# Kernel optimization log

Measured on AMD Instinct MI355X. Metric: run time of the kernel, lower is better.

Reference implementation:

```python
import jax, jax.numpy as jnp
import numpy as np

N_NODES = 100000
N_EDGES = 3200000
D_IN = 256
D_OUT = 256


def setup_inputs() -> dict:
    key = jax.random.key(0)
    k1, k2, k3, k4, k5 = jax.random.split(key, 5)
    # kaiming-uniform-like init for weight
    bound = float(np.sqrt(6.0 / D_IN))
    weight = jax.random.uniform(k1, (D_IN, D_OUT), dtype=jnp.float32, minval=-bound, maxval=bound)
    bias = jnp.zeros((D_OUT,), dtype=jnp.float32)
    input_feature = jax.random.normal(k2, (N_NODES, D_IN), dtype=jnp.float32)
    # sparse_poly in COO form: (row, col, val), typical normalized graph polynomial values
    edge_row = jax.random.randint(k3, (N_EDGES,), 0, N_NODES, dtype=jnp.int32)
    edge_col = jax.random.randint(k4, (N_EDGES,), 0, N_NODES, dtype=jnp.int32)
    edge_val = jax.random.uniform(k5, (N_EDGES,), dtype=jnp.float32)
    return {
        "input_feature": input_feature,
        "weight": weight,
        "bias": bias,
        "edge_val": edge_val,
        "edge_row": edge_row,
        "edge_col": edge_col,
    }


def reference(input_feature, weight, bias, edge_val, edge_row, edge_col):
    # support = X @ W  -> [N, D_OUT]
    support = input_feature @ weight
    # output = sparse_poly @ support  (COO SpMM):
    # gather source rows, scale by edge values, scatter-add into destination rows
    messages = edge_val[:, None] * support[edge_col]  # [E, D_OUT]
    output = jax.ops.segment_sum(messages, edge_row, num_segments=N_NODES)
    return output + bias
```

## Files before the change

### kernel.cpp

```cpp
#include <hip/hip_runtime.h>

#define D 256
#define GBM 128
#define WT_PITCH 264
#define BSH 9
#define RPB 512
#define NBMAX 256
#define TILE 4096

using bf16x8 = __attribute__((ext_vector_type(8))) short;
using f32x4  = __attribute__((ext_vector_type(4))) float;

static __device__ __forceinline__ unsigned short f2bf(float f) {
    unsigned u = __builtin_bit_cast(unsigned, f);
    return (unsigned short)((u + 0x7fffu + ((u >> 16) & 1u)) >> 16);
}
static __device__ __forceinline__ float as_f(unsigned u) {
    return __builtin_bit_cast(float, u);
}

__global__ void wt_kernel(const float* __restrict__ W, unsigned short* __restrict__ Wt) {
    int idx = blockIdx.x * blockDim.x + threadIdx.x;
    int n = idx & 255, k = idx >> 8;
    Wt[n * 256 + k] = f2bf(W[k * 256 + n]);
}

__global__ __launch_bounds__(512) void gemm_mfma(const float* __restrict__ X,
                                                 const unsigned short* __restrict__ Wt,
                                                 unsigned short* __restrict__ S, int N) {
    __shared__ unsigned short wlds[256 * WT_PITCH];

    for (int c = threadIdx.x; c < 8192; c += 512) {
        int n = c >> 5, kc = c & 31;
        uint4 v = *reinterpret_cast<const uint4*>(Wt + n * 256 + kc * 8);
        *reinterpret_cast<uint4*>(&wlds[n * WT_PITCH + kc * 8]) = v;
    }
    __syncthreads();

    const int lane = threadIdx.x & 63;
    const int wave = threadIdx.x >> 6;
    const int row0 = blockIdx.x * GBM + wave * 16;
    const int l16  = lane & 15;
    const int kgrp = lane >> 4;
    const int arow = min(row0 + l16, N - 1);
    const float* xp = X + (size_t)arow * 256 + kgrp * 8;

    f32x4 acc[16];
#pragma unroll
    for (int i = 0; i < 16; i++) acc[i] = (f32x4)(0.0f);

#pragma unroll
    for (int ks = 0; ks < 8; ks++) {
        float4 a0 = *reinterpret_cast<const float4*>(xp + ks * 32);
        float4 a1 = *reinterpret_cast<const float4*>(xp + ks * 32 + 4);
        bf16x8 af;
        af[0] = (short)f2bf(a0.x); af[1] = (short)f2bf(a0.y);
        af[2] = (short)f2bf(a0.z); af[3] = (short)f2bf(a0.w);
        af[4] = (short)f2bf(a1.x); af[5] = (short)f2bf(a1.y);
        af[6] = (short)f2bf(a1.z); af[7] = (short)f2bf(a1.w);
#pragma unroll
        for (int nt = 0; nt < 16; nt++) {
            bf16x8 bf = *reinterpret_cast<const bf16x8*>(
                &wlds[(nt * 16 + l16) * WT_PITCH + ks * 32 + kgrp * 8]);
            acc[nt] = __builtin_amdgcn_mfma_f32_16x16x32_bf16(af, bf, acc[nt], 0, 0, 0);
        }
    }

#pragma unroll
    for (int nt = 0; nt < 16; nt++) {
#pragma unroll
        for (int j = 0; j < 4; j++) {
            int r = row0 + kgrp * 4 + j;
            if (r < N) S[(size_t)r * 256 + nt * 16 + l16] = f2bf(acc[nt][j]);
        }
    }
}

__global__ __launch_bounds__(256) void bucket_hist(const int* __restrict__ rows,
                                                   int* __restrict__ bcounts,
                                                   int E, int NB) {
    __shared__ int lh[NBMAX];
    for (int i = threadIdx.x; i < NB; i += 256) lh[i] = 0;
    __syncthreads();
    const int stride = gridDim.x * 256;
    for (int e = blockIdx.x * 256 + threadIdx.x; e < E; e += stride)
        atomicAdd(&lh[rows[e] >> BSH], 1);
    __syncthreads();
    for (int i = threadIdx.x; i < NB; i += 256) {
        int v = lh[i];
        if (v) atomicAdd(&bcounts[i], v);
    }
}

__global__ __launch_bounds__(1024) void bscan_kernel(const int* __restrict__ bcounts,
                                                     int* __restrict__ boffs,
                                                     int* __restrict__ bcursor, int NB) {
    __shared__ int wsum[16];
    const int t = threadIdx.x, lane = t & 63, w = t >> 6;
    int x = (t < NB) ? bcounts[t] : 0;
    int s = x;
#pragma unroll
    for (int d = 1; d < 64; d <<= 1) {
        int y = __shfl_up(s, d);
        if (lane >= d) s += y;
    }
    if (lane == 63) wsum[w] = s;
    __syncthreads();
    if (w == 0) {
        int ws = (lane < 16) ? wsum[lane] : 0;
#pragma unroll
        for (int d = 1; d < 16; d <<= 1) {
            int y = __shfl_up(ws, d);
            if (lane >= d) ws += y;
        }
        if (lane < 16) wsum[lane] = ws;
    }
    __syncthreads();
    int excl = (w ? wsum[w - 1] : 0) + s - x;
    if (t < NB) { boffs[t] = excl; bcursor[t] = excl; }
}

__global__ __launch_bounds__(256) void partition_kernel(const int* __restrict__ rows,
                                                        const int* __restrict__ cols,
                                                        const float* __restrict__ vals,
                                                        int* __restrict__ bcursor,
                                                        int2* __restrict__ packed,
                                                        int E, int NB) {
    __shared__ int lh[NBMAX];
    __shared__ int gbase[NBMAX];
    const int t = threadIdx.x;
    const int e0 = blockIdx.x * TILE;

    for (int i = t; i < NB; i += 256) lh[i] = 0;
    __syncthreads();

    int bk[16], rk[16], pc[16], pv[16];
#pragma unroll
    for (int j = 0; j < 16; j++) {
        int idx = e0 + j * 256 + t;
        if (idx < E) {
            int r = rows[idx];
            bk[j] = r >> BSH;
            rk[j] = atomicAdd(&lh[bk[j]], 1);
            pc[j] = ((r & (RPB - 1)) << 17) | cols[idx];
            pv[j] = __float_as_int(vals[idx]);
        } else {
            bk[j] = -1;
        }
    }
    __syncthreads();

    for (int i = t; i < NB; i += 256) {
        int c = lh[i];
        gbase[i] = c ? atomicAdd(&bcursor[i], c) : 0;
    }
    __syncthreads();

#pragma unroll
    for (int j = 0; j < 16; j++) {
        if (bk[j] >= 0) {
            int2 p; p.x = pc[j]; p.y = pv[j];
            packed[(size_t)gbase[bk[j]] + rk[j]] = p;
        }
    }
}

__global__ __launch_bounds__(256) void bucket_scatter(const int2* __restrict__ packed,
                                                      const int* __restrict__ boffs,
                                                      const int* __restrict__ bcounts,
                                                      int* __restrict__ offs,
                                                      int* __restrict__ counts,
                                                      int2* __restrict__ cv, int N) {
    __shared__ int cnt[RPB];
    __shared__ int lofs[RPB];
    __shared__ int wsum[4];
    const int b = blockIdx.x, t = threadIdx.x;
    const int base = boffs[b], nb = bcounts[b];

    for (int i = t; i < RPB; i += 256) cnt[i] = 0;
    __syncthreads();
    for (int i = t; i < nb; i += 256)
        atomicAdd(&cnt[((unsigned)packed[base + i].x) >> 17], 1);
    __syncthreads();

    const int lane = t & 63, w = t >> 6;
    int a0 = cnt[2 * t], a1 = cnt[2 * t + 1];
    int s = a0 + a1;
    int ss = s;
#pragma unroll
    for (int d = 1; d < 64; d <<= 1) {
        int y = __shfl_up(ss, d);
        if (lane >= d) ss += y;
    }
    if (lane == 63) wsum[w] = ss;
    __syncthreads();
    int wex = 0;
    if (w > 0) wex += wsum[0];
    if (w > 1) wex += wsum[1];
    if (w > 2) wex += wsum[2];
    int excl = wex + ss - s;

    const int r0 = b << BSH;
    int r = r0 + 2 * t;
    if (r < N)     { offs[r]     = base + excl;      counts[r]     = a0; }
    if (r + 1 < N) { offs[r + 1] = base + excl + a0; counts[r + 1] = a1; }
    lofs[2 * t]     = excl;
    lofs[2 * t + 1] = excl + a0;
    __syncthreads();

    for (int i = t; i < nb; i += 256) {
        int2 p = packed[base + i];
        int lr = ((unsigned)p.x) >> 17;
        int pos = base + atomicAdd(&lofs[lr], 1);
        int2 o;
        o.x = p.x & 0x1FFFF;
        o.y = p.y;
        cv[pos] = o;
    }
}

__global__ __launch_bounds__(256) void spmm_kernel(const unsigned short* __restrict__ S,
                                                   const int* __restrict__ offs,
                                                   const int* __restrict__ counts,
                                                   const int2* __restrict__ cv,
                                                   const float* __restrict__ bias,
                                                   float* __restrict__ out, int N) {
    const int lane = threadIdx.x & 63;
    const int r = blockIdx.x * 4 + (threadIdx.x >> 6);
    if (r >= N) return;
    const char* Sb = reinterpret_cast<const char*>(S);

    float4 acc = { 0.f, 0.f, 0.f, 0.f };
    int i = offs[r];
    const int end = i + counts[r];

#define GATHER(c, v)                                                              \
    {                                                                             \
        uint2 sv = *reinterpret_cast<const uint2*>(Sb + ((size_t)(c) << 9) + (lane << 3)); \
        acc.x += (v) * as_f(sv.x << 16);                                          \
        acc.y += (v) * as_f(sv.x & 0xffff0000u);                                  \
        acc.z += (v) * as_f(sv.y << 16);                                          \
        acc.w += (v) * as_f(sv.y & 0xffff0000u);                                  \
    }

    for (; i + 3 < end; i += 4) {
        int2 e0 = cv[i], e1 = cv[i + 1], e2 = cv[i + 2], e3 = cv[i + 3];
        GATHER(e0.x, as_f((unsigned)e0.y));
        GATHER(e1.x, as_f((unsigned)e1.y));
        GATHER(e2.x, as_f((unsigned)e2.y));
        GATHER(e3.x, as_f((unsigned)e3.y));
    }
    for (; i < end; i++) {
        int2 e0 = cv[i];
        GATHER(e0.x, as_f((unsigned)e0.y));
    }
#undef GATHER

    float4 b = reinterpret_cast<const float4*>(bias)[lane];
    float4 o = { acc.x + b.x, acc.y + b.y, acc.z + b.z, acc.w + b.w };
    reinterpret_cast<float4*>(out)[(size_t)r * 64 + lane] = o;
}

extern "C" void kernel_launch(void* const* d_in, const int* in_sizes, int n_in,
                              void* d_out, int out_size, void* d_ws, size_t ws_size,
                              hipStream_t stream) {
    const float* X     = (const float*)d_in[0];
    const float* W     = (const float*)d_in[1];
    const float* bias  = (const float*)d_in[2];
    const float* evals = (const float*)d_in[3];
    const int*   erow  = (const int*)d_in[4];
    const int*   ecol  = (const int*)d_in[5];
    float* out = (float*)d_out;

    const int N = in_sizes[0] / D;
    const int E = in_sizes[3];
    const int NB = (N + RPB - 1) >> BSH;

    char* ws = (char*)d_ws;
    size_t off = 0;
    auto alloc = [&](size_t bytes) {
        void* p = ws + off;
        off += (bytes + 255) & ~(size_t)255;
        return p;
    };
    unsigned short* S  = (unsigned short*)alloc((size_t)N * D * sizeof(unsigned short));
    unsigned short* Wt = (unsigned short*)alloc((size_t)D * D * sizeof(unsigned short));
    int* bcounts = (int*)alloc((size_t)NB * sizeof(int));
    int* boffs   = (int*)alloc((size_t)NB * sizeof(int));
    int* bcursor = (int*)alloc((size_t)NB * sizeof(int));
    int* offs    = (int*)alloc((size_t)N * sizeof(int));
    int* counts  = (int*)alloc((size_t)N * sizeof(int));
    int2* packed = (int2*)alloc((size_t)E * sizeof(int2));
    int2* cv     = (int2*)alloc((size_t)E * sizeof(int2));

    wt_kernel<<<(D * D) / 256, 256, 0, stream>>>(W, Wt);
    gemm_mfma<<<(N + GBM - 1) / GBM, 512, 0, stream>>>(X, Wt, S, N);
    hipMemsetAsync(bcounts, 0, (size_t)NB * sizeof(int), stream);
    bucket_hist<<<1024, 256, 0, stream>>>(erow, bcounts, E, NB);
    bscan_kernel<<<1, 1024, 0, stream>>>(bcounts, boffs, bcursor, NB);
    partition_kernel<<<(E + TILE - 1) / TILE, 256, 0, stream>>>(erow, ecol, evals, bcursor,
                                                                packed, E, NB);
    bucket_scatter<<<NB, 256, 0, stream>>>(packed, boffs, bcounts, offs, counts, cv, N);
    spmm_kernel<<<(N + 3) / 4, 256, 0, stream>>>(S, offs, counts, cv, bias, out, N);
}
```

Measured before the change: 413.2 us.

## Drop GEMM LDS staging, fold memset, widen bucket scatter and unroll SpMM

The GEMM no longer stages the bf16 weight into a 135KB shared-memory tile. Each wave now reads B fragments straight from global/L2, and blocks shrink to 256 threads covering 64 rows, which should let more blocks fit per CU. The bcounts memset is folded into wt_kernel, bucket_scatter runs 1024 threads with a two-level scan, and the SpMM gather loop is unrolled by 8 to put more loads in flight. The risk is heavier L2 traffic for the weight reads in the GEMM.

```diff
diff --git a/kernel.cpp b/kernel.cpp
--- a/kernel.cpp
+++ b/kernel.cpp
@@ -1,7 +1,6 @@
 #include <hip/hip_runtime.h>
 
 #define D 256
-#define GBM 128
 #define WT_PITCH 264
 #define BSH 9
 #define RPB 512
@@ -19,31 +18,25 @@
     return __builtin_bit_cast(float, u);
 }
 
-__global__ void wt_kernel(const float* __restrict__ W, unsigned short* __restrict__ Wt) {
+__global__ void wt_kernel(const float* __restrict__ W, unsigned short* __restrict__ Wt,
+                          int* __restrict__ bcounts, int NB) {
     int idx = blockIdx.x * blockDim.x + threadIdx.x;
     int n = idx & 255, k = idx >> 8;
     Wt[n * 256 + k] = f2bf(W[k * 256 + n]);
-}
-
-__global__ __launch_bounds__(512) void gemm_mfma(const float* __restrict__ X,
+    if (blockIdx.x == 0 && threadIdx.x < NB) bcounts[threadIdx.x] = 0;
+}
+
+__global__ __launch_bounds__(256) void gemm_mfma(const float* __restrict__ X,
                                                  const unsigned short* __restrict__ Wt,
                                                  unsigned short* __restrict__ S, int N) {
-    __shared__ unsigned short wlds[256 * WT_PITCH];
-
-    for (int c = threadIdx.x; c < 8192; c += 512) {
-        int n = c >> 5, kc = c & 31;
-        uint4 v = *reinterpret_cast<const uint4*>(Wt + n * 256 + kc * 8);
-        *reinterpret_cast<uint4*>(&wlds[n * WT_PITCH + kc * 8]) = v;
-    }
-    __syncthreads();
-
     const int lane = threadIdx.x & 63;
     const int wave = threadIdx.x >> 6;
-    const int row0 = blockIdx.x * GBM + wave * 16;
+    const int row0 = blockIdx.x * 64 + wave * 16;
     const int l16  = lane & 15;
     const int kgrp = lane >> 4;
     const int arow = min(row0 + l16, N - 1);
     const float* xp = X + (size_t)arow * 256 + kgrp * 8;
+    const unsigned short* wp = Wt + l16 * 256 + kgrp * 8;
 
     f32x4 acc[16];
 #pragma unroll
@@ -61,7 +54,7 @@
 #pragma unroll
         for (int nt = 0; nt < 16; nt++) {
             bf16x8 bf = *reinterpret_cast<const bf16x8*>(
-                &wlds[(nt * 16 + l16) * WT_PITCH + ks * 32 + kgrp * 8]);
+                wp + nt * 16 * 256 + ks * 32);
             acc[nt] = __builtin_amdgcn_mfma_f32_16x16x32_bf16(af, bf, acc[nt], 0, 0, 0);
         }
     }
@@ -165,50 +158,55 @@
     }
 }
 
-__global__ __launch_bounds__(256) void bucket_scatter(const int2* __restrict__ packed,
-                                                      const int* __restrict__ boffs,
-                                                      const int* __restrict__ bcounts,
-                                                      int* __restrict__ offs,
-                                                      int* __restrict__ counts,
-                                                      int2* __restrict__ cv, int N) {
+__global__ __launch_bounds__(1024) void bucket_scatter(const int2* __restrict__ packed,
+                                                       const int* __restrict__ boffs,
+                                                       const int* __restrict__ bcounts,
+                                                       int* __restrict__ offs,
+                                                       int* __restrict__ counts,
+                                                       int2* __restrict__ cv, int N) {
     __shared__ int cnt[RPB];
     __shared__ int lofs[RPB];
-    __shared__ int wsum[4];
+    __shared__ int wsum[16];
     const int b = blockIdx.x, t = threadIdx.x;
     const int base = boffs[b], nb = bcounts[b];
-
-    for (int i = t; i < RPB; i += 256) cnt[i] = 0;
-    __syncthreads();
-    for (int i = t; i < nb; i += 256)
+    const int lane = t & 63, w = t >> 6;
+
+    for (int i = t; i < RPB; i += 1024) cnt[i] = 0;
+    __syncthreads();
+    for (int i = t; i < nb; i += 1024)
         atomicAdd(&cnt[((unsigned)packed[base + i].x) >> 17], 1);
     __syncthreads();
 
-    const int lane = t & 63, w = t >> 6;
-    int a0 = cnt[2 * t], a1 = cnt[2 * t + 1];
-    int s = a0 + a1;
-    int ss = s;
+    int x = (t < RPB) ? cnt[t] : 0;
+    int s = x;
 #pragma unroll
     for (int d = 1; d < 64; d <<= 1) {
-        int y = __shfl_up(ss, d);
-        if (lane >= d) ss += y;
-    }
-    if (lane == 63) wsum[w] = ss;
-    __syncthreads();
-    int wex = 0;
-    if (w > 0) wex += wsum[0];
-    if (w > 1) wex += wsum[1];
-    if (w > 2) wex += wsum[2];
-    int excl = wex + ss - s;
+        int y = __shfl_up(s, d);
+        if (lane >= d) s += y;
+    }
+    if (lane == 63) wsum[w] = s;
+    __syncthreads();
+    if (w == 0) {
+        int ws = (lane < 16) ? wsum[lane] : 0;
+#pragma unroll
+        for (int d = 1; d < 16; d <<= 1) {
+            int y = __shfl_up(ws, d);
+            if (lane >= d) ws += y;
+        }
+        if (lane < 16) wsum[lane] = ws;
+    }
+    __syncthreads();
+    int excl = (w ? wsum[w - 1] : 0) + s - x;
 
     const int r0 = b << BSH;
-    int r = r0 + 2 * t;
-    if (r < N)     { offs[r]     = base + excl;      counts[r]     = a0; }
-    if (r + 1 < N) { offs[r + 1] = base + excl + a0; counts[r + 1] = a1; }
-    lofs[2 * t]     = excl;
-    lofs[2 * t + 1] = excl + a0;
-    __syncthreads();
-
-    for (int i = t; i < nb; i += 256) {
+    if (t < RPB) {
+        int r = r0 + t;
+        if (r < N) { offs[r] = base + excl; counts[r] = x; }
+        lofs[t] = excl;
+    }
+    __syncthreads();
+
+    for (int i = t; i < nb; i += 1024) {
         int2 p = packed[base + i];
         int lr = ((unsigned)p.x) >> 17;
         int pos = base + atomicAdd(&lofs[lr], 1);
@@ -243,14 +241,24 @@
         acc.w += (v) * as_f(sv.y & 0xffff0000u);                                  \
     }
 
-    for (; i + 3 < end; i += 4) {
-        int2 e0 = cv[i], e1 = cv[i + 1], e2 = cv[i + 2], e3 = cv[i + 3];
+    for (; i + 7 < end; i += 8) {
+        int2 e0 = cv[i],     e1 = cv[i + 1], e2 = cv[i + 2], e3 = cv[i + 3];
+        int2 e4 = cv[i + 4], e5 = cv[i + 5], e6 = cv[i + 6], e7 = cv[i + 7];
         GATHER(e0.x, as_f((unsigned)e0.y));
         GATHER(e1.x, as_f((unsigned)e1.y));
         GATHER(e2.x, as_f((unsigned)e2.y));
         GATHER(e3.x, as_f((unsigned)e3.y));
-    }
-    for (; i < end; i++) {
+        GATHER(e4.x, as_f((unsigned)e4.y));
+        GATHER(e5.x, as_f((unsigned)e5.y));
+        GATHER(e6.x, as_f((unsigned)e6.y));
+        GATHER(e7.x, as_f((unsigned)e7.y));
+    }
+    for (; i + 1 < end; i += 2) {
+        int2 e0 = cv[i], e1 = cv[i + 1];
+        GATHER(e0.x, as_f((unsigned)e0.y));
+        GATHER(e1.x, as_f((unsigned)e1.y));
+    }
+    if (i < end) {
         int2 e0 = cv[i];
         GATHER(e0.x, as_f((unsigned)e0.y));
     }
@@ -274,7 +282,7 @@
 
     const int N = in_sizes[0] / D;
     const int E = in_sizes[3];
-    const int NB = (N + RPB - 1) >> BSH;
+    const int NB = ((N - 1) >> BSH) + 1;
 
     char* ws = (char*)d_ws;
     size_t off = 0;
@@ -293,13 +301,12 @@
     int2* packed = (int2*)alloc((size_t)E * sizeof(int2));
     int2* cv     = (int2*)alloc((size_t)E * sizeof(int2));
 
-    wt_kernel<<<(D * D) / 256, 256, 0, stream>>>(W, Wt);
-    gemm_mfma<<<(N + GBM - 1) / GBM, 512, 0, stream>>>(X, Wt, S, N);
-    hipMemsetAsync(bcounts, 0, (size_t)NB * sizeof(int), stream);
+    wt_kernel<<<(D * D) / 256, 256, 0, stream>>>(W, Wt, bcounts, NB);
+    gemm_mfma<<<(N + 63) / 64, 256, 0, stream>>>(X, Wt, S, N);
     bucket_hist<<<1024, 256, 0, stream>>>(erow, bcounts, E, NB);
     bscan_kernel<<<1, 1024, 0, stream>>>(bcounts, boffs, bcursor, NB);
     partition_kernel<<<(E + TILE - 1) / TILE, 256, 0, stream>>>(erow, ecol, evals, bcursor,
                                                                 packed, E, NB);
-    bucket_scatter<<<NB, 256, 0, stream>>>(packed, boffs, bcounts, offs, counts, cv, N);
+    bucket_scatter<<<NB, 1024, 0, stream>>>(packed, boffs, bcounts, offs, counts, cv, N);
     spmm_kernel<<<(N + 3) / 4, 256, 0, stream>>>(S, offs, counts, cv, bias, out, N);
 }
```

Result: slower. 470.7 us (+13.9%).

## Fuse bucket histogram into GEMM, add nontemporal loads/stores, unroll SpMM by 8

Applied to the files above, without the earlier changes.

The bucket histogram moves into the GEMM kernel, and the bcounts memset moves into the weight-transpose kernel, removing two launches. The GEMM block doubles to 1024 threads covering 256 rows each, and X is read with nontemporal loads. The SpMM kernel loads edges as packed 64-bit nontemporal values, unrolls by 8 instead of 4, and writes output with nontemporal stores. Larger GEMM blocks mean fewer blocks per CU and fewer blocks overall, and the histogram work now runs after the GEMM inside the same block, which could lengthen the critical path.

```diff
diff --git a/kernel.cpp b/kernel.cpp
--- a/kernel.cpp
+++ b/kernel.cpp
@@ -1,7 +1,7 @@
 #include <hip/hip_runtime.h>
 
 #define D 256
-#define GBM 128
+#define GBM 256
 #define WT_PITCH 264
 #define BSH 9
 #define RPB 512
@@ -19,22 +19,29 @@
     return __builtin_bit_cast(float, u);
 }
 
-__global__ void wt_kernel(const float* __restrict__ W, unsigned short* __restrict__ Wt) {
+__global__ void wt_kernel(const float* __restrict__ W, unsigned short* __restrict__ Wt,
+                          int* __restrict__ bcounts, int NB) {
     int idx = blockIdx.x * blockDim.x + threadIdx.x;
     int n = idx & 255, k = idx >> 8;
     Wt[n * 256 + k] = f2bf(W[k * 256 + n]);
-}
-
-__global__ __launch_bounds__(512) void gemm_mfma(const float* __restrict__ X,
-                                                 const unsigned short* __restrict__ Wt,
-                                                 unsigned short* __restrict__ S, int N) {
+    if (blockIdx.x == 0 && threadIdx.x < NB) bcounts[threadIdx.x] = 0;
+}
+
+__global__ __launch_bounds__(1024) void gemm_mfma(const float* __restrict__ X,
+                                                  const unsigned short* __restrict__ Wt,
+                                                  unsigned short* __restrict__ S, int N,
+                                                  const int* __restrict__ erow,
+                                                  int* __restrict__ bcounts,
+                                                  int E, int NB) {
     __shared__ unsigned short wlds[256 * WT_PITCH];
-
-    for (int c = threadIdx.x; c < 8192; c += 512) {
+    __shared__ int lh[NBMAX];
+
+    for (int c = threadIdx.x; c < 8192; c += 1024) {
         int n = c >> 5, kc = c & 31;
         uint4 v = *reinterpret_cast<const uint4*>(Wt + n * 256 + kc * 8);
         *reinterpret_cast<uint4*>(&wlds[n * WT_PITCH + kc * 8]) = v;
     }
+    for (int i = threadIdx.x; i < NB; i += 1024) lh[i] = 0;
     __syncthreads();
 
     const int lane = threadIdx.x & 63;
@@ -51,13 +58,13 @@
 
 #pragma unroll
     for (int ks = 0; ks < 8; ks++) {
-        float4 a0 = *reinterpret_cast<const float4*>(xp + ks * 32);
-        float4 a1 = *reinterpret_cast<const float4*>(xp + ks * 32 + 4);
+        f32x4 a0 = __builtin_nontemporal_load(reinterpret_cast<const f32x4*>(xp + ks * 32));
+        f32x4 a1 = __builtin_nontemporal_load(reinterpret_cast<const f32x4*>(xp + ks * 32 + 4));
         bf16x8 af;
-        af[0] = (short)f2bf(a0.x); af[1] = (short)f2bf(a0.y);
-        af[2] = (short)f2bf(a0.z); af[3] = (short)f2bf(a0.w);
-        af[4] = (short)f2bf(a1.x); af[5] = (short)f2bf(a1.y);
-        af[6] = (short)f2bf(a1.z); af[7] = (short)f2bf(a1.w);
+        af[0] = (short)f2bf(a0[0]); af[1] = (short)f2bf(a0[1]);
+        af[2] = (short)f2bf(a0[2]); af[3] = (short)f2bf(a0[3]);
+        af[4] = (short)f2bf(a1[0]); af[5] = (short)f2bf(a1[1]);
+        af[6] = (short)f2bf(a1[2]); af[7] = (short)f2bf(a1[3]);
 #pragma unroll
         for (int nt = 0; nt < 16; nt++) {
             bf16x8 bf = *reinterpret_cast<const bf16x8*>(
@@ -74,19 +81,12 @@
             if (r < N) S[(size_t)r * 256 + nt * 16 + l16] = f2bf(acc[nt][j]);
         }
     }
-}
-
-__global__ __launch_bounds__(256) void bucket_hist(const int* __restrict__ rows,
-                                                   int* __restrict__ bcounts,
-                                                   int E, int NB) {
-    __shared__ int lh[NBMAX];
-    for (int i = threadIdx.x; i < NB; i += 256) lh[i] = 0;
-    __syncthreads();
-    const int stride = gridDim.x * 256;
-    for (int e = blockIdx.x * 256 + threadIdx.x; e < E; e += stride)
-        atomicAdd(&lh[rows[e] >> BSH], 1);
-    __syncthreads();
-    for (int i = threadIdx.x; i < NB; i += 256) {
+
+    const int stride = gridDim.x * 1024;
+    for (int e = blockIdx.x * 1024 + threadIdx.x; e < E; e += stride)
+        atomicAdd(&lh[erow[e] >> BSH], 1);
+    __syncthreads();
+    for (int i = threadIdx.x; i < NB; i += 1024) {
         int v = lh[i];
         if (v) atomicAdd(&bcounts[i], v);
     }
@@ -176,6 +176,7 @@
     __shared__ int wsum[4];
     const int b = blockIdx.x, t = threadIdx.x;
     const int base = boffs[b], nb = bcounts[b];
+    const int lane = t & 63, w = t >> 6;
 
     for (int i = t; i < RPB; i += 256) cnt[i] = 0;
     __syncthreads();
@@ -183,7 +184,6 @@
         atomicAdd(&cnt[((unsigned)packed[base + i].x) >> 17], 1);
     __syncthreads();
 
-    const int lane = t & 63, w = t >> 6;
     int a0 = cnt[2 * t], a1 = cnt[2 * t + 1];
     int s = a0 + a1;
     int ss = s;
@@ -229,36 +229,46 @@
     const int r = blockIdx.x * 4 + (threadIdx.x >> 6);
     if (r >= N) return;
     const char* Sb = reinterpret_cast<const char*>(S);
+    const unsigned long long* cve = reinterpret_cast<const unsigned long long*>(cv);
 
     float4 acc = { 0.f, 0.f, 0.f, 0.f };
     int i = offs[r];
     const int end = i + counts[r];
 
-#define GATHER(c, v)                                                              \
+#define LOADE(k) __builtin_nontemporal_load(cve + (k))
+#define GATHER(e)                                                                 \
     {                                                                             \
-        uint2 sv = *reinterpret_cast<const uint2*>(Sb + ((size_t)(c) << 9) + (lane << 3)); \
-        acc.x += (v) * as_f(sv.x << 16);                                          \
-        acc.y += (v) * as_f(sv.x & 0xffff0000u);                                  \
-        acc.z += (v) * as_f(sv.y << 16);                                          \
-        acc.w += (v) * as_f(sv.y & 0xffff0000u);                                  \
-    }
-
-    for (; i + 3 < end; i += 4) {
-        int2 e0 = cv[i], e1 = cv[i + 1], e2 = cv[i + 2], e3 = cv[i + 3];
-        GATHER(e0.x, as_f((unsigned)e0.y));
-        GATHER(e1.x, as_f((unsigned)e1.y));
-        GATHER(e2.x, as_f((unsigned)e2.y));
-        GATHER(e3.x, as_f((unsigned)e3.y));
-    }
-    for (; i < end; i++) {
-        int2 e0 = cv[i];
-        GATHER(e0.x, as_f((unsigned)e0.y));
+        unsigned c = (unsigned)((e) & 0xffffffffu);                               \
+        float v = as_f((unsigned)((e) >> 32));                                    \
+        uint2 sv = *reinterpret_cast<const uint2*>(Sb + ((size_t)c << 9) + (lane << 3)); \
+        acc.x += v * as_f(sv.x << 16);                                            \
+        acc.y += v * as_f(sv.x & 0xffff0000u);                                    \
+        acc.z += v * as_f(sv.y << 16);                                            \
+        acc.w += v * as_f(sv.y & 0xffff0000u);                                    \
+    }
+
+    for (; i + 7 < end; i += 8) {
+        unsigned long long e0 = LOADE(i),     e1 = LOADE(i + 1);
+        unsigned long long e2 = LOADE(i + 2), e3 = LOADE(i + 3);
+        unsigned long long e4 = LOADE(i + 4), e5 = LOADE(i + 5);
+        unsigned long long e6 = LOADE(i + 6), e7 = LOADE(i + 7);
+        GATHER(e0); GATHER(e1); GATHER(e2); GATHER(e3);
+        GATHER(e4); GATHER(e5); GATHER(e6); GATHER(e7);
+    }
+    for (; i + 1 < end; i += 2) {
+        unsigned long long e0 = LOADE(i), e1 = LOADE(i + 1);
+        GATHER(e0); GATHER(e1);
+    }
+    if (i < end) {
+        unsigned long long e0 = LOADE(i);
+        GATHER(e0);
     }
 #undef GATHER
+#undef LOADE
 
     float4 b = reinterpret_cast<const float4*>(bias)[lane];
-    float4 o = { acc.x + b.x, acc.y + b.y, acc.z + b.z, acc.w + b.w };
-    reinterpret_cast<float4*>(out)[(size_t)r * 64 + lane] = o;
+    f32x4 o = { acc.x + b.x, acc.y + b.y, acc.z + b.z, acc.w + b.w };
+    __builtin_nontemporal_store(o, reinterpret_cast<f32x4*>(out) + (size_t)r * 64 + lane);
 }
 
 extern "C" void kernel_launch(void* const* d_in, const int* in_sizes, int n_in,
@@ -274,7 +284,7 @@
 
     const int N = in_sizes[0] / D;
     const int E = in_sizes[3];
-    const int NB = (N + RPB - 1) >> BSH;
+    const int NB = ((N - 1) >> BSH) + 1;
 
     char* ws = (char*)d_ws;
     size_t off = 0;
@@ -293,10 +303,8 @@
     int2* packed = (int2*)alloc((size_t)E * sizeof(int2));
     int2* cv     = (int2*)alloc((size_t)E * sizeof(int2));
 
-    wt_kernel<<<(D * D) / 256, 256, 0, stream>>>(W, Wt);
-    gemm_mfma<<<(N + GBM - 1) / GBM, 512, 0, stream>>>(X, Wt, S, N);
-    hipMemsetAsync(bcounts, 0, (size_t)NB * sizeof(int), stream);
-    bucket_hist<<<1024, 256, 0, stream>>>(erow, bcounts, E, NB);
+    wt_kernel<<<(D * D) / 256, 256, 0, stream>>>(W, Wt, bcounts, NB);
+    gemm_mfma<<<(N + GBM - 1) / GBM, 1024, 0, stream>>>(X, Wt, S, N, erow, bcounts, E, NB);
     bscan_kernel<<<1, 1024, 0, stream>>>(bcounts, boffs, bcursor, NB);
     partition_kernel<<<(E + TILE - 1) / TILE, 256, 0, stream>>>(erow, ecol, evals, bcursor,
                                                                 packed, E, NB);
```

Result: faster. 379.6 us (-8.1%).
